# Performance work log

Hardware: AMD Instinct MI355X
Metric: run time of the kernel (lower is better)

The kernel has to match this reference:

```python
import jax, jax.numpy as jnp
import numpy as np

SEQ_LEN = 131072
NUM_NODES = 256
NUM_CAUSES = 16
NUM_FEATURES = 100
NUM_OUTPUTS = 1
NOISE_STD = 0.01


def _build_dag_mask(N, C, p, rng):
    # upper-triangular random adjacency; roots (0..C-1) have no parents;
    # every non-root gets at least one parent (mirrors _build_random_dag)
    A = (rng.random((N, N)) < p) & np.triu(np.ones((N, N), bool), k=1)
    A[:, :C] = False
    for j in range(C, N):
        if not A[:j, j].any():
            A[rng.integers(0, j), j] = True
    return A.astype(np.int32)


def setup_inputs() -> dict:
    key = jax.random.key(0)
    k1, k2, k3 = jax.random.split(key, 3)
    rng = np.random.default_rng(0)
    S, N, C = SEQ_LEN, NUM_NODES, NUM_CAUSES
    causes = jax.random.normal(k1, (S, C), dtype=jnp.float32)
    W = jax.random.normal(k2, (N, N), dtype=jnp.float32)  # edge weights w_ij ~ N(0,1)
    eps = jax.random.normal(k3, (S, N - C), dtype=jnp.float32)  # unit noise, scaled by NOISE_STD
    mask = jnp.asarray(_build_dag_mask(N, C, 0.3, rng))
    act_id = jnp.asarray(rng.integers(0, 4, size=(N - C,)), dtype=jnp.int32)
    # y from a sink-like last node; X from sorted sample of remaining non-root nodes
    y_idx = jnp.asarray([N - 1], dtype=jnp.int64)
    X_idx = jnp.asarray(np.sort(rng.choice(np.arange(C, N - 1), size=NUM_FEATURES, replace=False)), dtype=jnp.int64)
    return {"causes": causes, "W": W, "eps": eps, "mask": mask, "act_id": act_id, "X_idx": X_idx, "y_idx": y_idx}


def reference(causes, W, eps, mask, act_id, X_idx, y_idx):
    S, C = causes.shape
    N = W.shape[0]
    Wm = W * mask.astype(W.dtype)                      # [N,N] masked edge weights (parent i -> node j)
    vals0 = jnp.zeros((S, N), W.dtype).at[:, :C].set(causes)
    Wcols = Wm.T[C:]                                   # [N-C, N] incoming-weight rows per non-root node
    eps_t = eps.T                                      # [N-C, S]
    branches = [lambda z: z, jnp.tanh, jax.nn.relu, jax.nn.sigmoid]

    def step(carry, xs):
        vals, idx = carry
        w_col, e, a = xs
        z = vals @ w_col + jnp.float32(NOISE_STD) * e  # weighted parent sum + noise, [S]
        v = jax.lax.switch(a, branches, z)
        vals = vals.at[:, idx].set(v)
        return (vals, idx + 1), None

    (vals, _), _ = jax.lax.scan(step, (vals0, jnp.int32(C)), (Wcols, eps_t, act_id))
    X = vals[:, X_idx]                                 # [S, num_features]
    y = vals[:, y_idx]                                 # [S, 1]
    bad = jnp.isnan(X).any() | jnp.isnan(y).any()
    X = jnp.where(bad, jnp.float32(0.0), X)
    y = jnp.where(bad, jnp.float32(-100.0), y)
    return X, y[:, 0]                                  # num_outputs == 1 -> squeeze
```

## Files before the change

kernel.cpp:

```cpp
#include <hip/hip_runtime.h>
#include <hip/hip_bf16.h>
#include <hip/hip_fp16.h>


typedef _Float16 half8 __attribute__((ext_vector_type(8)));
typedef float    f32x4 __attribute__((ext_vector_type(4)));

constexpr int S_LEN    = 131072;
constexpr int N_NODES  = 256;
constexpr int N_CAUSES = 16;
constexpr int N_COMP   = 240;
constexpr int N_FEAT   = 100;
constexpr float NOISE  = 0.01f;
constexpr float VSC    = 0.0625f;
constexpr float VSCI   = 16.0f;

constexpr int KE_tab[16]  = {0,32,64,64,96,96,128,128,160,160,192,192,224,224,256,256};
constexpr int OFF_tab[16] = {0,0,1024,3072,5120,8192,11264,15360,19456,24576,29696,
                             35840,41984,49152,56320,64512};

__constant__ int c_KE[16]  = {0,32,64,64,96,96,128,128,160,160,192,192,224,224,256,256};
__constant__ int c_OFF[16] = {0,0,1024,3072,5120,8192,11264,15360,19456,24576,29696,
                              35840,41984,49152,56320,64512};

__device__ _Float16 g_WT[72704];
__device__ float    g_Wtri[15 * 256];

__device__ __forceinline__ bool sniff_binary64(const void* p) {
    const unsigned* u = (const unsigned*)p;
    bool ok = true;
    for (int i = 0; i < 64; ++i) ok = ok && (u[i] <= 1u);
    return ok;
}
__device__ __forceinline__ bool sniff_is_bf16(const void* p) {
    const unsigned* u = (const unsigned*)p;
    bool ok = true;
    for (int i = 0; i < 16; ++i) {
        unsigned e = ((u[i] << 16) >> 23) & 0xffu;
        ok = ok && (e >= 100u) && (e <= 132u);
    }
    return ok;
}
__device__ __forceinline__ float bflo(unsigned u) { return __uint_as_float(u << 16); }
__device__ __forceinline__ float bfhi(unsigned u) { return __uint_as_float(u & 0xffff0000u); }

__device__ __forceinline__ void load16(const void* base, long long off, bool isbf, float* o) {
    if (isbf) {
        const uint4* p = (const uint4*)((const unsigned short*)base + off);
        uint4 a = p[0], b = p[1];
        o[0]=bflo(a.x); o[1]=bfhi(a.x); o[2]=bflo(a.y); o[3]=bfhi(a.y);
        o[4]=bflo(a.z); o[5]=bfhi(a.z); o[6]=bflo(a.w); o[7]=bfhi(a.w);
        o[8]=bflo(b.x); o[9]=bfhi(b.x); o[10]=bflo(b.y); o[11]=bfhi(b.y);
        o[12]=bflo(b.z); o[13]=bfhi(b.z); o[14]=bflo(b.w); o[15]=bfhi(b.w);
    } else {
        const float4* p = (const float4*)((const float*)base + off);
        float4 x0=p[0], x1=p[1], x2=p[2], x3=p[3];
        o[0]=x0.x; o[1]=x0.y; o[2]=x0.z; o[3]=x0.w;
        o[4]=x1.x; o[5]=x1.y; o[6]=x1.z; o[7]=x1.w;
        o[8]=x2.x; o[9]=x2.y; o[10]=x2.z; o[11]=x2.w;
        o[12]=x3.x; o[13]=x3.y; o[14]=x3.z; o[15]=x3.w;
    }
}

__device__ __forceinline__ float hw_exp2(float x) {
    float r; asm("v_exp_f32 %0, %1" : "=v"(r) : "v"(x)); return r;
}
__device__ __forceinline__ float hw_rcp(float x) {
    float r; asm("v_rcp_f32 %0, %1" : "=v"(r) : "v"(x)); return r;
}
__device__ __forceinline__ float fast_tanh(float x) {
    float t = hw_exp2(x * 2.88539008177792681f);
    return 1.0f - 2.0f * hw_rcp(t + 1.0f);
}
__device__ __forceinline__ float fast_sigmoid(float x) {
    return hw_rcp(1.0f + hw_exp2(x * -1.44269504088896341f));
}

__global__ void prep_kernel(const void* __restrict__ A, const void* __restrict__ B) {
    __shared__ int s_mA, s_wbf;
    if (threadIdx.x == 0) {
        s_mA  = sniff_binary64(A) ? 1 : 0;
        s_wbf = sniff_is_bf16(s_mA ? B : A) ? 1 : 0;
    }
    __syncthreads();
    const int*  maskp = (const int*)(s_mA ? A : B);
    const void* Wp    = s_mA ? B : A;
    const int k = blockIdx.x + 1, j0 = 16 * k, KE = c_KE[k], OFF = c_OFF[k];
    const int tid = threadIdx.x;

    for (int n = 0; n < 16; ++n) {
        const int j = j0 + n;
        for (int kk = tid; kk < KE; kk += 256) {
            const int gi = kk * N_NODES + j;
            float w = 0.0f;
            if (maskp[gi])
                w = s_wbf ? __bfloat162float(((const __hip_bfloat16*)Wp)[gi])
                          : ((const float*)Wp)[gi];
            const _Float16 hi = (_Float16)w;
            const _Float16 lo = (_Float16)(w - (float)hi);
            g_WT[OFF + n * KE + kk]           = hi;
            g_WT[OFF + 16 * KE + n * KE + kk] = lo;
        }
    }
    {
        const int l = tid >> 4, i = tid & 15;
        const int gi = (j0 + l) * N_NODES + (j0 + i);
        float w = 0.0f;
        if (l < i && maskp[gi])
            w = s_wbf ? __bfloat162float(((const __hip_bfloat16*)Wp)[gi])
                      : ((const float*)Wp)[gi];
        g_Wtri[(k - 1) * 256 + tid] = w;
    }
}

#define MFMA16(a, b, c) __builtin_amdgcn_mfma_f32_16x16x32_f16((a), (b), (c), 0, 0, 0)

template<int K>
__device__ __forceinline__ void do_chunk(
    const int lane, const long long sg,
    const void* __restrict__ eps, const bool ebf,
    half8 (&vf)[2][8],
    float* __restrict__ Zbuf, _Float16* __restrict__ stag,
    const short* __restrict__ xpos, const int* __restrict__ act_id,
    float* __restrict__ wsX,
    float* __restrict__ outX, float* __restrict__ outY, const int yi)
{
    constexpr int j0  = 16 * K;
    constexpr int KE  = KE_tab[K];
    constexpr int NST = KE / 32;
    constexpr int OFF = OFF_tab[K];

    const int mrow = lane & 15;
    const int quad = lane >> 4;

    float ev[16];
    if (lane < 32)
        load16(eps, sg * (long long)N_COMP + (j0 - N_CAUSES), ebf, ev);

    const _Float16* __restrict__ bp = g_WT + OFF + mrow * KE + (quad << 3);

    f32x4 acc0h = {0.f,0.f,0.f,0.f}, acc0l = {0.f,0.f,0.f,0.f};
    f32x4 acc1h = {0.f,0.f,0.f,0.f}, acc1l = {0.f,0.f,0.f,0.f};

    #pragma unroll
    for (int t = 0; t < NST; ++t) {
        const half8 bh = *(const half8*)(bp + (t << 5));
        const half8 bl = *(const half8*)(bp + 16 * KE + (t << 5));
        acc0h = MFMA16(vf[0][t], bh, acc0h);
        acc1h = MFMA16(vf[1][t], bh, acc1h);
        acc0l = MFMA16(vf[0][t], bl, acc0l);
        acc1l = MFMA16(vf[1][t], bl, acc1l);
    }

    {
        const int r0 = quad << 2;
        #pragma unroll
        for (int r = 0; r < 4; ++r) {
            Zbuf[(r0 + r)      * 21 + mrow] = (acc0h[r] + acc0l[r]) * VSCI;
            Zbuf[(16 + r0 + r) * 21 + mrow] = (acc1h[r] + acc1l[r]) * VSCI;
        }
    }
    __builtin_amdgcn_wave_barrier();

    if (lane < 32) {
        float zz[16];
        #pragma unroll
        for (int i = 0; i < 16; ++i)
            zz[i] = Zbuf[lane * 21 + i] + NOISE * ev[i];

        const float* __restrict__ tri = g_Wtri + (K - 1) * 256;
        half8 h0, h1;
        #pragma unroll
        for (int i = 0; i < 16; ++i) {
            float z = zz[i];
            const int a = act_id[j0 - N_CAUSES + i];
            if (a == 1)      z = fast_tanh(z);
            else if (a == 2) z = fmaxf(z, 0.0f);
            else if (a == 3) z = fast_sigmoid(z);
            if (i < 8) h0[i] = (_Float16)(z * VSC);
            else       h1[i - 8] = (_Float16)(z * VSC);
            const int xp = xpos[j0 - N_CAUSES + i];
            if (xp >= 0) {
                if (wsX) wsX[(long long)xp * S_LEN + sg] = z;
                else     outX[xp] = z;
            }
            if (j0 + i == yi) outY[sg] = z;
            #pragma unroll
            for (int j = i + 1; j < 16; ++j)
                zz[j] += tri[(i << 4) + j] * z;
        }
        *(half8*)(stag + lane * 24)     = h0;
        *(half8*)(stag + lane * 24 + 8) = h1;
    }
    __builtin_amdgcn_wave_barrier();

    constexpr int TT = K >> 1;
    constexpr int HB = (K & 1) << 1;
    const int hq = lane >> 4;
    if (hq == HB || hq == HB + 1) {
        const int boff = (hq - HB) << 3;
        #pragma unroll
        for (int q = 0; q < 2; ++q)
            vf[q][TT] = *(const half8*)(stag + (q * 16 + (lane & 15)) * 24 + boff);
    }
    __builtin_amdgcn_wave_barrier();
}

__global__ __launch_bounds__(64, 4)
void scm_kernel(const void* __restrict__ causes,
                const void* __restrict__ eps,
                const int* __restrict__ act_id,
                const void* __restrict__ xidx_raw,
                const int* __restrict__ yidx_raw,
                float* __restrict__ out,
                float* __restrict__ wsX,
                long long ybase) {
    __shared__ __align__(16) float    Zbuf[32 * 21];
    __shared__ __align__(16) _Float16 stag[32 * 24];
    __shared__ short xpos[N_COMP];

    const int lane = threadIdx.x;
    const long long sg = (long long)blockIdx.x * 32 + lane;

    for (int t = lane; t < N_COMP; t += 64) xpos[t] = -1;
    const unsigned long long* x64 = (const unsigned long long*)xidx_raw;
    const int*                x32 = (const int*)xidx_raw;
    const bool is64 = ((x64[0] >> 32) == 0ull);
    __builtin_amdgcn_wave_barrier();
    for (int f = lane; f < N_FEAT; f += 64) {
        const int ix = is64 ? (int)x64[f] : x32[f];
        xpos[ix - N_CAUSES] = (short)f;
    }
    __builtin_amdgcn_wave_barrier();
    const int yi  = yidx_raw[0];
    const bool cbf = sniff_is_bf16(causes);
    const bool ebf = sniff_is_bf16(eps);

    half8 vz;
    #pragma unroll
    for (int e = 0; e < 8; ++e) vz[e] = (_Float16)0.0f;
    half8 vf[2][8];
    #pragma unroll
    for (int q = 0; q < 2; ++q) {
        #pragma unroll
        for (int t = 0; t < 8; ++t) vf[q][t] = vz;
    }

    if (lane < 32) {
        float cv[16];
        load16(causes, sg * (long long)N_CAUSES, cbf, cv);
        half8 c0, c1;
        #pragma unroll
        for (int i = 0; i < 8; ++i) {
            c0[i] = (_Float16)(cv[i] * VSC);
            c1[i] = (_Float16)(cv[8 + i] * VSC);
        }
        *(half8*)(stag + lane * 24)     = c0;
        *(half8*)(stag + lane * 24 + 8) = c1;
    }
    __builtin_amdgcn_wave_barrier();
    {
        const int hq = lane >> 4;
        if (hq < 2) {
            #pragma unroll
            for (int q = 0; q < 2; ++q)
                vf[q][0] = *(const half8*)(stag + (q * 16 + (lane & 15)) * 24 + (hq << 3));
        }
    }
    __builtin_amdgcn_wave_barrier();

    float* outX = out + sg * N_FEAT;
    float* outY = out + ybase;

    do_chunk< 1>(lane, sg, eps, ebf, vf, Zbuf, stag, xpos, act_id, wsX, outX, outY, yi);
    do_chunk< 2>(lane, sg, eps, ebf, vf, Zbuf, stag, xpos, act_id, wsX, outX, outY, yi);
    do_chunk< 3>(lane, sg, eps, ebf, vf, Zbuf, stag, xpos, act_id, wsX, outX, outY, yi);
    do_chunk< 4>(lane, sg, eps, ebf, vf, Zbuf, stag, xpos, act_id, wsX, outX, outY, yi);
    do_chunk< 5>(lane, sg, eps, ebf, vf, Zbuf, stag, xpos, act_id, wsX, outX, outY, yi);
    do_chunk< 6>(lane, sg, eps, ebf, vf, Zbuf, stag, xpos, act_id, wsX, outX, outY, yi);
    do_chunk< 7>(lane, sg, eps, ebf, vf, Zbuf, stag, xpos, act_id, wsX, outX, outY, yi);
    do_chunk< 8>(lane, sg, eps, ebf, vf, Zbuf, stag, xpos, act_id, wsX, outX, outY, yi);
    do_chunk< 9>(lane, sg, eps, ebf, vf, Zbuf, stag, xpos, act_id, wsX, outX, outY, yi);
    do_chunk<10>(lane, sg, eps, ebf, vf, Zbuf, stag, xpos, act_id, wsX, outX, outY, yi);
    do_chunk<11>(lane, sg, eps, ebf, vf, Zbuf, stag, xpos, act_id, wsX, outX, outY, yi);
    do_chunk<12>(lane, sg, eps, ebf, vf, Zbuf, stag, xpos, act_id, wsX, outX, outY, yi);
    do_chunk<13>(lane, sg, eps, ebf, vf, Zbuf, stag, xpos, act_id, wsX, outX, outY, yi);
    do_chunk<14>(lane, sg, eps, ebf, vf, Zbuf, stag, xpos, act_id, wsX, outX, outY, yi);
    do_chunk<15>(lane, sg, eps, ebf, vf, Zbuf, stag, xpos, act_id, wsX, outX, outY, yi);
}

__global__ __launch_bounds__(256)
void xpose_kernel(const float* __restrict__ ws, float* __restrict__ out) {
    __shared__ float tile[64 * 100];
    const int tid = threadIdx.x;
    const long long s0 = (long long)blockIdx.x * 64;
    const int f = tid >> 6;
    const int s = tid & 63;
    #pragma unroll
    for (int g = 0; g < 25; ++g) {
        const int ff = f + g * 4;
        tile[s * 100 + ff] = ws[(long long)ff * S_LEN + s0 + s];
    }
    __syncthreads();
    float4* o4 = (float4*)(out + s0 * N_FEAT);
    const float4* t4 = (const float4*)tile;
    #pragma unroll
    for (int g = 0; g < 7; ++g) {
        const int idx = g * 256 + tid;
        if (idx < 1600) o4[idx] = t4[idx];
    }
}

extern "C" void kernel_launch(void* const* d_in, const int* in_sizes, int n_in,
                              void* d_out, int out_size, void* d_ws, size_t ws_size,
                              hipStream_t stream) {
    int ic = 0, iw = 1, ie = 2, im = 3, ia = 4, ix = 5, iy = 6;
    int c = -1, e = -1, a = -1, x = -1, y = -1, m1 = -1, m2 = -1;
    for (int i = 0; i < n_in; ++i) {
        switch (in_sizes[i]) {
            case S_LEN * N_CAUSES:   c = i; break;
            case S_LEN * N_COMP:     e = i; break;
            case N_COMP:             a = i; break;
            case N_FEAT:             x = i; break;
            case 1:                  y = i; break;
            case N_NODES * N_NODES:  (m1 < 0 ? m1 : m2) = i; break;
        }
    }
    if (c >= 0 && e >= 0 && a >= 0 && x >= 0 && y >= 0 && m1 >= 0 && m2 >= 0) {
        ic = c; ie = e; ia = a; ix = x; iy = y; iw = m1; im = m2;
    }

    const void* causes = d_in[ic];
    const void* TA     = d_in[iw];
    const void* TB     = d_in[im];
    const void* eps    = d_in[ie];
    const int*  act_id = (const int*)d_in[ia];
    const void* xidx   = d_in[ix];
    const int*  yidx   = (const int*)d_in[iy];
    float*      out    = (float*)d_out;
    const long long ybase = (long long)out_size - S_LEN;

    const bool usews = ws_size >= (size_t)N_FEAT * S_LEN * sizeof(float);
    float* wsX = usews ? (float*)d_ws : nullptr;

    prep_kernel<<<15, 256, 0, stream>>>(TA, TB);
    scm_kernel<<<S_LEN / 32, 64, 0, stream>>>(causes, eps, act_id, xidx, yidx,
                                              out, wsX, ybase);
    if (usews)
        xpose_kernel<<<S_LEN / 64, 256, 0, stream>>>(wsX, out);
}
```

Baseline: 353.4 us.

## Roll chunk loop with padded full-width weights and vectorize transpose kernel

The 15 unrolled per-chunk template instantiations become a single rolled loop. Weights are stored in a uniform zero-padded 256-wide layout so each chunk always runs 8 MFMA steps instead of a variable count. This shrinks code size and instruction-cache pressure, at the price of extra MFMA work on zero-padded columns for early chunks. The transpose kernel now reads float4 vectors and pads its shared tile to cut bank conflicts.

```diff
diff --git a/kernel.cpp b/kernel.cpp
--- a/kernel.cpp
+++ b/kernel.cpp
@@ -15,15 +15,7 @@
 constexpr float VSC    = 0.0625f;
 constexpr float VSCI   = 16.0f;
 
-constexpr int KE_tab[16]  = {0,32,64,64,96,96,128,128,160,160,192,192,224,224,256,256};
-constexpr int OFF_tab[16] = {0,0,1024,3072,5120,8192,11264,15360,19456,24576,29696,
-                             35840,41984,49152,56320,64512};
-
-__constant__ int c_KE[16]  = {0,32,64,64,96,96,128,128,160,160,192,192,224,224,256,256};
-__constant__ int c_OFF[16] = {0,0,1024,3072,5120,8192,11264,15360,19456,24576,29696,
-                              35840,41984,49152,56320,64512};
-
-__device__ _Float16 g_WT[72704];
+__device__ _Float16 g_WT2[15 * 2 * 16 * 256];
 __device__ float    g_Wtri[15 * 256];
 
 __device__ __forceinline__ bool sniff_binary64(const void* p) {
@@ -85,22 +77,19 @@
     __syncthreads();
     const int*  maskp = (const int*)(s_mA ? A : B);
     const void* Wp    = s_mA ? B : A;
-    const int k = blockIdx.x + 1, j0 = 16 * k, KE = c_KE[k], OFF = c_OFF[k];
+    const int k = blockIdx.x + 1, j0 = 16 * k;
     const int tid = threadIdx.x;
 
     for (int n = 0; n < 16; ++n) {
-        const int j = j0 + n;
-        for (int kk = tid; kk < KE; kk += 256) {
-            const int gi = kk * N_NODES + j;
-            float w = 0.0f;
-            if (maskp[gi])
-                w = s_wbf ? __bfloat162float(((const __hip_bfloat16*)Wp)[gi])
-                          : ((const float*)Wp)[gi];
-            const _Float16 hi = (_Float16)w;
-            const _Float16 lo = (_Float16)(w - (float)hi);
-            g_WT[OFF + n * KE + kk]           = hi;
-            g_WT[OFF + 16 * KE + n * KE + kk] = lo;
-        }
+        const int gi = tid * N_NODES + (j0 + n);
+        float w = 0.0f;
+        if (maskp[gi])
+            w = s_wbf ? __bfloat162float(((const __hip_bfloat16*)Wp)[gi])
+                      : ((const float*)Wp)[gi];
+        const _Float16 hi = (_Float16)w;
+        const _Float16 lo = (_Float16)(w - (float)hi);
+        g_WT2[(k - 1) * 8192 + n * 256 + tid]        = hi;
+        g_WT2[(k - 1) * 8192 + 4096 + n * 256 + tid] = lo;
     }
     {
         const int l = tid >> 4, i = tid & 15;
@@ -114,97 +103,6 @@
 }
 
 #define MFMA16(a, b, c) __builtin_amdgcn_mfma_f32_16x16x32_f16((a), (b), (c), 0, 0, 0)
-
-template<int K>
-__device__ __forceinline__ void do_chunk(
-    const int lane, const long long sg,
-    const void* __restrict__ eps, const bool ebf,
-    half8 (&vf)[2][8],
-    float* __restrict__ Zbuf, _Float16* __restrict__ stag,
-    const short* __restrict__ xpos, const int* __restrict__ act_id,
-    float* __restrict__ wsX,
-    float* __restrict__ outX, float* __restrict__ outY, const int yi)
-{
-    constexpr int j0  = 16 * K;
-    constexpr int KE  = KE_tab[K];
-    constexpr int NST = KE / 32;
-    constexpr int OFF = OFF_tab[K];
-
-    const int mrow = lane & 15;
-    const int quad = lane >> 4;
-
-    float ev[16];
-    if (lane < 32)
-        load16(eps, sg * (long long)N_COMP + (j0 - N_CAUSES), ebf, ev);
-
-    const _Float16* __restrict__ bp = g_WT + OFF + mrow * KE + (quad << 3);
-
-    f32x4 acc0h = {0.f,0.f,0.f,0.f}, acc0l = {0.f,0.f,0.f,0.f};
-    f32x4 acc1h = {0.f,0.f,0.f,0.f}, acc1l = {0.f,0.f,0.f,0.f};
-
-    #pragma unroll
-    for (int t = 0; t < NST; ++t) {
-        const half8 bh = *(const half8*)(bp + (t << 5));
-        const half8 bl = *(const half8*)(bp + 16 * KE + (t << 5));
-        acc0h = MFMA16(vf[0][t], bh, acc0h);
-        acc1h = MFMA16(vf[1][t], bh, acc1h);
-        acc0l = MFMA16(vf[0][t], bl, acc0l);
-        acc1l = MFMA16(vf[1][t], bl, acc1l);
-    }
-
-    {
-        const int r0 = quad << 2;
-        #pragma unroll
-        for (int r = 0; r < 4; ++r) {
-            Zbuf[(r0 + r)      * 21 + mrow] = (acc0h[r] + acc0l[r]) * VSCI;
-            Zbuf[(16 + r0 + r) * 21 + mrow] = (acc1h[r] + acc1l[r]) * VSCI;
-        }
-    }
-    __builtin_amdgcn_wave_barrier();
-
-    if (lane < 32) {
-        float zz[16];
-        #pragma unroll
-        for (int i = 0; i < 16; ++i)
-            zz[i] = Zbuf[lane * 21 + i] + NOISE * ev[i];
-
-        const float* __restrict__ tri = g_Wtri + (K - 1) * 256;
-        half8 h0, h1;
-        #pragma unroll
-        for (int i = 0; i < 16; ++i) {
-            float z = zz[i];
-            const int a = act_id[j0 - N_CAUSES + i];
-            if (a == 1)      z = fast_tanh(z);
-            else if (a == 2) z = fmaxf(z, 0.0f);
-            else if (a == 3) z = fast_sigmoid(z);
-            if (i < 8) h0[i] = (_Float16)(z * VSC);
-            else       h1[i - 8] = (_Float16)(z * VSC);
-            const int xp = xpos[j0 - N_CAUSES + i];
-            if (xp >= 0) {
-                if (wsX) wsX[(long long)xp * S_LEN + sg] = z;
-                else     outX[xp] = z;
-            }
-            if (j0 + i == yi) outY[sg] = z;
-            #pragma unroll
-            for (int j = i + 1; j < 16; ++j)
-                zz[j] += tri[(i << 4) + j] * z;
-        }
-        *(half8*)(stag + lane * 24)     = h0;
-        *(half8*)(stag + lane * 24 + 8) = h1;
-    }
-    __builtin_amdgcn_wave_barrier();
-
-    constexpr int TT = K >> 1;
-    constexpr int HB = (K & 1) << 1;
-    const int hq = lane >> 4;
-    if (hq == HB || hq == HB + 1) {
-        const int boff = (hq - HB) << 3;
-        #pragma unroll
-        for (int q = 0; q < 2; ++q)
-            vf[q][TT] = *(const half8*)(stag + (q * 16 + (lane & 15)) * 24 + boff);
-    }
-    __builtin_amdgcn_wave_barrier();
-}
 
 __global__ __launch_bounds__(64, 4)
 void scm_kernel(const void* __restrict__ causes,
@@ -236,6 +134,9 @@
     const bool cbf = sniff_is_bf16(causes);
     const bool ebf = sniff_is_bf16(eps);
 
+    const int mrow = lane & 15;
+    const int quad = lane >> 4;
+
     half8 vz;
     #pragma unroll
     for (int e = 0; e < 8; ++e) vz[e] = (_Float16)0.0f;
@@ -259,55 +160,139 @@
         *(half8*)(stag + lane * 24 + 8) = c1;
     }
     __builtin_amdgcn_wave_barrier();
-    {
-        const int hq = lane >> 4;
-        if (hq < 2) {
-            #pragma unroll
-            for (int q = 0; q < 2; ++q)
-                vf[q][0] = *(const half8*)(stag + (q * 16 + (lane & 15)) * 24 + (hq << 3));
-        }
+    if (quad < 2) {
+        #pragma unroll
+        for (int q = 0; q < 2; ++q)
+            vf[q][0] = *(const half8*)(stag + (q * 16 + mrow) * 24 + (quad << 3));
     }
     __builtin_amdgcn_wave_barrier();
 
     float* outX = out + sg * N_FEAT;
     float* outY = out + ybase;
 
-    do_chunk< 1>(lane, sg, eps, ebf, vf, Zbuf, stag, xpos, act_id, wsX, outX, outY, yi);
-    do_chunk< 2>(lane, sg, eps, ebf, vf, Zbuf, stag, xpos, act_id, wsX, outX, outY, yi);
-    do_chunk< 3>(lane, sg, eps, ebf, vf, Zbuf, stag, xpos, act_id, wsX, outX, outY, yi);
-    do_chunk< 4>(lane, sg, eps, ebf, vf, Zbuf, stag, xpos, act_id, wsX, outX, outY, yi);
-    do_chunk< 5>(lane, sg, eps, ebf, vf, Zbuf, stag, xpos, act_id, wsX, outX, outY, yi);
-    do_chunk< 6>(lane, sg, eps, ebf, vf, Zbuf, stag, xpos, act_id, wsX, outX, outY, yi);
-    do_chunk< 7>(lane, sg, eps, ebf, vf, Zbuf, stag, xpos, act_id, wsX, outX, outY, yi);
-    do_chunk< 8>(lane, sg, eps, ebf, vf, Zbuf, stag, xpos, act_id, wsX, outX, outY, yi);
-    do_chunk< 9>(lane, sg, eps, ebf, vf, Zbuf, stag, xpos, act_id, wsX, outX, outY, yi);
-    do_chunk<10>(lane, sg, eps, ebf, vf, Zbuf, stag, xpos, act_id, wsX, outX, outY, yi);
-    do_chunk<11>(lane, sg, eps, ebf, vf, Zbuf, stag, xpos, act_id, wsX, outX, outY, yi);
-    do_chunk<12>(lane, sg, eps, ebf, vf, Zbuf, stag, xpos, act_id, wsX, outX, outY, yi);
-    do_chunk<13>(lane, sg, eps, ebf, vf, Zbuf, stag, xpos, act_id, wsX, outX, outY, yi);
-    do_chunk<14>(lane, sg, eps, ebf, vf, Zbuf, stag, xpos, act_id, wsX, outX, outY, yi);
-    do_chunk<15>(lane, sg, eps, ebf, vf, Zbuf, stag, xpos, act_id, wsX, outX, outY, yi);
+    #define UPD(TT, HB)                                                        \
+        if (quad == (HB) || quad == (HB) + 1) {                                \
+            const int boff = (quad - (HB)) << 3;                               \
+            vf[0][TT] = *(const half8*)(stag + mrow * 24 + boff);              \
+            vf[1][TT] = *(const half8*)(stag + (16 + mrow) * 24 + boff);       \
+        }
+
+    #pragma unroll 1
+    for (int k = 1; k <= 15; ++k) {
+        const int j0 = k << 4;
+
+        float ev[16];
+        if (lane < 32)
+            load16(eps, sg * (long long)N_COMP + (j0 - N_CAUSES), ebf, ev);
+
+        const _Float16* __restrict__ bp =
+            g_WT2 + (k - 1) * 8192 + mrow * 256 + (quad << 3);
+
+        f32x4 acc0h = {0.f,0.f,0.f,0.f}, acc0l = {0.f,0.f,0.f,0.f};
+        f32x4 acc1h = {0.f,0.f,0.f,0.f}, acc1l = {0.f,0.f,0.f,0.f};
+
+        #pragma unroll
+        for (int t = 0; t < 8; ++t) {
+            const half8 bh = *(const half8*)(bp + (t << 5));
+            const half8 bl = *(const half8*)(bp + 4096 + (t << 5));
+            acc0h = MFMA16(vf[0][t], bh, acc0h);
+            acc1h = MFMA16(vf[1][t], bh, acc1h);
+            acc0l = MFMA16(vf[0][t], bl, acc0l);
+            acc1l = MFMA16(vf[1][t], bl, acc1l);
+        }
+
+        {
+            const int r0 = quad << 2;
+            #pragma unroll
+            for (int r = 0; r < 4; ++r) {
+                Zbuf[(r0 + r)      * 21 + mrow] = (acc0h[r] + acc0l[r]) * VSCI;
+                Zbuf[(16 + r0 + r) * 21 + mrow] = (acc1h[r] + acc1l[r]) * VSCI;
+            }
+        }
+        __builtin_amdgcn_wave_barrier();
+
+        if (lane < 32) {
+            float zz[16];
+            #pragma unroll
+            for (int i = 0; i < 16; ++i)
+                zz[i] = Zbuf[lane * 21 + i] + NOISE * ev[i];
+
+            const float* __restrict__ tri = g_Wtri + (k - 1) * 256;
+            half8 h0, h1;
+            #pragma unroll
+            for (int i = 0; i < 16; ++i) {
+                float z = zz[i];
+                const int a = act_id[j0 - N_CAUSES + i];
+                if (a == 1)      z = fast_tanh(z);
+                else if (a == 2) z = fmaxf(z, 0.0f);
+                else if (a == 3) z = fast_sigmoid(z);
+                if (i < 8) h0[i] = (_Float16)(z * VSC);
+                else       h1[i - 8] = (_Float16)(z * VSC);
+                const int xp = xpos[j0 - N_CAUSES + i];
+                if (xp >= 0) {
+                    if (wsX) wsX[(long long)xp * S_LEN + sg] = z;
+                    else     outX[xp] = z;
+                }
+                if (j0 + i == yi) outY[sg] = z;
+                #pragma unroll
+                for (int j = i + 1; j < 16; ++j)
+                    zz[j] += tri[(i << 4) + j] * z;
+            }
+            *(half8*)(stag + lane * 24)     = h0;
+            *(half8*)(stag + lane * 24 + 8) = h1;
+        }
+        __builtin_amdgcn_wave_barrier();
+
+        switch (k) {
+            case  1: UPD(0, 2); break;
+            case  2: UPD(1, 0); break;
+            case  3: UPD(1, 2); break;
+            case  4: UPD(2, 0); break;
+            case  5: UPD(2, 2); break;
+            case  6: UPD(3, 0); break;
+            case  7: UPD(3, 2); break;
+            case  8: UPD(4, 0); break;
+            case  9: UPD(4, 2); break;
+            case 10: UPD(5, 0); break;
+            case 11: UPD(5, 2); break;
+            case 12: UPD(6, 0); break;
+            case 13: UPD(6, 2); break;
+            case 14: UPD(7, 0); break;
+            case 15: UPD(7, 2); break;
+        }
+        __builtin_amdgcn_wave_barrier();
+    }
+    #undef UPD
 }
 
 __global__ __launch_bounds__(256)
 void xpose_kernel(const float* __restrict__ ws, float* __restrict__ out) {
-    __shared__ float tile[64 * 100];
+    __shared__ float tile[64 * 108];
     const int tid = threadIdx.x;
     const long long s0 = (long long)blockIdx.x * 64;
-    const int f = tid >> 6;
-    const int s = tid & 63;
-    #pragma unroll
-    for (int g = 0; g < 25; ++g) {
-        const int ff = f + g * 4;
-        tile[s * 100 + ff] = ws[(long long)ff * S_LEN + s0 + s];
-    }
-    __syncthreads();
-    float4* o4 = (float4*)(out + s0 * N_FEAT);
-    const float4* t4 = (const float4*)tile;
     #pragma unroll
     for (int g = 0; g < 7; ++g) {
         const int idx = g * 256 + tid;
-        if (idx < 1600) o4[idx] = t4[idx];
+        if (idx < 1600) {
+            const int ff = idx >> 4;
+            const int sl = idx & 15;
+            const float4 v = *(const float4*)(ws + (long long)ff * S_LEN + s0 + sl * 4);
+            tile[(sl * 4 + 0) * 108 + ff] = v.x;
+            tile[(sl * 4 + 1) * 108 + ff] = v.y;
+            tile[(sl * 4 + 2) * 108 + ff] = v.z;
+            tile[(sl * 4 + 3) * 108 + ff] = v.w;
+        }
+    }
+    __syncthreads();
+    #pragma unroll
+    for (int g = 0; g < 7; ++g) {
+        const int idx = g * 256 + tid;
+        if (idx < 1600) {
+            const int s = idx / 25;
+            const int j = idx % 25;
+            const float4 v = *(const float4*)(tile + s * 108 + j * 4);
+            *(float4*)(out + (s0 + s) * N_FEAT + j * 4) = v;
+        }
     }
 }
 
```

Result: slower. 403.7 us (+14.2%).

## Pack activation/destination metadata, branchless activations, unconditional workspace stores, vectorized transpose

Applied to the files above, without the earlier changes.

Packs each node's activation id and output destination into one shared short. The workspace path now stores every node unconditionally: feature rows, the y row, or a trash row. This removes per-node branches and the y-index compare. Activations are computed branchlessly via selects, the explicit wave barriers are dropped, and the transpose kernel now uses float4 loads, a padded tile, and also copies y. The trade-off is extra work per node, since all three activations are evaluated and stores go to the trash row. It also needs a slightly larger workspace and relies on implicit ordering within a single wave.

```diff
diff --git a/kernel.cpp b/kernel.cpp
--- a/kernel.cpp
+++ b/kernel.cpp
@@ -14,6 +14,10 @@
 constexpr float NOISE  = 0.01f;
 constexpr float VSC    = 0.0625f;
 constexpr float VSCI   = 16.0f;
+
+constexpr int ROW_Y  = 100;
+constexpr int ROW_TR = 101;
+constexpr int WS_ROWS = 102;
 
 constexpr int KE_tab[16]  = {0,32,64,64,96,96,128,128,160,160,192,192,224,224,256,256};
 constexpr int OFF_tab[16] = {0,0,1024,3072,5120,8192,11264,15360,19456,24576,29696,
@@ -121,9 +125,9 @@
     const void* __restrict__ eps, const bool ebf,
     half8 (&vf)[2][8],
     float* __restrict__ Zbuf, _Float16* __restrict__ stag,
-    const short* __restrict__ xpos, const int* __restrict__ act_id,
+    const short* __restrict__ meta,
     float* __restrict__ wsX,
-    float* __restrict__ outX, float* __restrict__ outY, const int yi)
+    float* __restrict__ outX, float* __restrict__ outY)
 {
     constexpr int j0  = 16 * K;
     constexpr int KE  = KE_tab[K];
@@ -160,7 +164,6 @@
             Zbuf[(16 + r0 + r) * 21 + mrow] = (acc1h[r] + acc1l[r]) * VSCI;
         }
     }
-    __builtin_amdgcn_wave_barrier();
 
     if (lane < 32) {
         float zz[16];
@@ -170,40 +173,54 @@
 
         const float* __restrict__ tri = g_Wtri + (K - 1) * 256;
         half8 h0, h1;
-        #pragma unroll
-        for (int i = 0; i < 16; ++i) {
-            float z = zz[i];
-            const int a = act_id[j0 - N_CAUSES + i];
-            if (a == 1)      z = fast_tanh(z);
-            else if (a == 2) z = fmaxf(z, 0.0f);
-            else if (a == 3) z = fast_sigmoid(z);
-            if (i < 8) h0[i] = (_Float16)(z * VSC);
-            else       h1[i - 8] = (_Float16)(z * VSC);
-            const int xp = xpos[j0 - N_CAUSES + i];
-            if (xp >= 0) {
-                if (wsX) wsX[(long long)xp * S_LEN + sg] = z;
-                else     outX[xp] = z;
+        if (wsX) {
+            #pragma unroll
+            for (int i = 0; i < 16; ++i) {
+                float z = zz[i];
+                const int m = meta[j0 - N_CAUSES + i];
+                const int a = m & 3;
+                const float th = fast_tanh(z);
+                const float re = fmaxf(z, 0.0f);
+                const float sgm = fast_sigmoid(z);
+                z = (a == 1) ? th : (a == 2) ? re : (a == 3) ? sgm : z;
+                if (i < 8) h0[i] = (_Float16)(z * VSC);
+                else       h1[i - 8] = (_Float16)(z * VSC);
+                wsX[((long long)(m >> 2)) * S_LEN + sg] = z;
+                #pragma unroll
+                for (int j = i + 1; j < 16; ++j)
+                    zz[j] += tri[(i << 4) + j] * z;
             }
-            if (j0 + i == yi) outY[sg] = z;
+        } else {
             #pragma unroll
-            for (int j = i + 1; j < 16; ++j)
-                zz[j] += tri[(i << 4) + j] * z;
+            for (int i = 0; i < 16; ++i) {
+                float z = zz[i];
+                const int m = meta[j0 - N_CAUSES + i];
+                const int a = m & 3;
+                if (a == 1)      z = fast_tanh(z);
+                else if (a == 2) z = fmaxf(z, 0.0f);
+                else if (a == 3) z = fast_sigmoid(z);
+                if (i < 8) h0[i] = (_Float16)(z * VSC);
+                else       h1[i - 8] = (_Float16)(z * VSC);
+                const int dr = m >> 2;
+                if (dr < ROW_Y)       outX[dr] = z;
+                else if (dr == ROW_Y) outY[sg] = z;
+                #pragma unroll
+                for (int j = i + 1; j < 16; ++j)
+                    zz[j] += tri[(i << 4) + j] * z;
+            }
         }
         *(half8*)(stag + lane * 24)     = h0;
         *(half8*)(stag + lane * 24 + 8) = h1;
     }
-    __builtin_amdgcn_wave_barrier();
 
     constexpr int TT = K >> 1;
     constexpr int HB = (K & 1) << 1;
-    const int hq = lane >> 4;
-    if (hq == HB || hq == HB + 1) {
-        const int boff = (hq - HB) << 3;
+    if (quad == HB || quad == HB + 1) {
+        const int boff = (quad - HB) << 3;
         #pragma unroll
         for (int q = 0; q < 2; ++q)
-            vf[q][TT] = *(const half8*)(stag + (q * 16 + (lane & 15)) * 24 + boff);
-    }
-    __builtin_amdgcn_wave_barrier();
+            vf[q][TT] = *(const half8*)(stag + (q * 16 + mrow) * 24 + boff);
+    }
 }
 
 __global__ __launch_bounds__(64, 4)
@@ -217,24 +234,30 @@
                 long long ybase) {
     __shared__ __align__(16) float    Zbuf[32 * 21];
     __shared__ __align__(16) _Float16 stag[32 * 24];
-    __shared__ short xpos[N_COMP];
+    __shared__ short meta[N_COMP];
 
     const int lane = threadIdx.x;
     const long long sg = (long long)blockIdx.x * 32 + lane;
 
-    for (int t = lane; t < N_COMP; t += 64) xpos[t] = -1;
+    for (int t = lane; t < N_COMP; t += 64) meta[t] = -1;
     const unsigned long long* x64 = (const unsigned long long*)xidx_raw;
     const int*                x32 = (const int*)xidx_raw;
     const bool is64 = ((x64[0] >> 32) == 0ull);
-    __builtin_amdgcn_wave_barrier();
     for (int f = lane; f < N_FEAT; f += 64) {
         const int ix = is64 ? (int)x64[f] : x32[f];
-        xpos[ix - N_CAUSES] = (short)f;
-    }
-    __builtin_amdgcn_wave_barrier();
-    const int yi  = yidx_raw[0];
+        meta[ix - N_CAUSES] = (short)f;
+    }
+    const int yi = yidx_raw[0];
+    for (int n = lane; n < N_COMP; n += 64) {
+        const int xp = meta[n];
+        const int dst = (n + N_CAUSES == yi) ? ROW_Y : (xp >= 0 ? xp : ROW_TR);
+        meta[n] = (short)((act_id[n] & 3) | (dst << 2));
+    }
     const bool cbf = sniff_is_bf16(causes);
     const bool ebf = sniff_is_bf16(eps);
+
+    const int mrow = lane & 15;
+    const int quad = lane >> 4;
 
     half8 vz;
     #pragma unroll
@@ -258,56 +281,65 @@
         *(half8*)(stag + lane * 24)     = c0;
         *(half8*)(stag + lane * 24 + 8) = c1;
     }
-    __builtin_amdgcn_wave_barrier();
-    {
-        const int hq = lane >> 4;
-        if (hq < 2) {
-            #pragma unroll
-            for (int q = 0; q < 2; ++q)
-                vf[q][0] = *(const half8*)(stag + (q * 16 + (lane & 15)) * 24 + (hq << 3));
-        }
-    }
-    __builtin_amdgcn_wave_barrier();
+    if (quad < 2) {
+        #pragma unroll
+        for (int q = 0; q < 2; ++q)
+            vf[q][0] = *(const half8*)(stag + (q * 16 + mrow) * 24 + (quad << 3));
+    }
 
     float* outX = out + sg * N_FEAT;
     float* outY = out + ybase;
 
-    do_chunk< 1>(lane, sg, eps, ebf, vf, Zbuf, stag, xpos, act_id, wsX, outX, outY, yi);
-    do_chunk< 2>(lane, sg, eps, ebf, vf, Zbuf, stag, xpos, act_id, wsX, outX, outY, yi);
-    do_chunk< 3>(lane, sg, eps, ebf, vf, Zbuf, stag, xpos, act_id, wsX, outX, outY, yi);
-    do_chunk< 4>(lane, sg, eps, ebf, vf, Zbuf, stag, xpos, act_id, wsX, outX, outY, yi);
-    do_chunk< 5>(lane, sg, eps, ebf, vf, Zbuf, stag, xpos, act_id, wsX, outX, outY, yi);
-    do_chunk< 6>(lane, sg, eps, ebf, vf, Zbuf, stag, xpos, act_id, wsX, outX, outY, yi);
-    do_chunk< 7>(lane, sg, eps, ebf, vf, Zbuf, stag, xpos, act_id, wsX, outX, outY, yi);
-    do_chunk< 8>(lane, sg, eps, ebf, vf, Zbuf, stag, xpos, act_id, wsX, outX, outY, yi);
-    do_chunk< 9>(lane, sg, eps, ebf, vf, Zbuf, stag, xpos, act_id, wsX, outX, outY, yi);
-    do_chunk<10>(lane, sg, eps, ebf, vf, Zbuf, stag, xpos, act_id, wsX, outX, outY, yi);
-    do_chunk<11>(lane, sg, eps, ebf, vf, Zbuf, stag, xpos, act_id, wsX, outX, outY, yi);
-    do_chunk<12>(lane, sg, eps, ebf, vf, Zbuf, stag, xpos, act_id, wsX, outX, outY, yi);
-    do_chunk<13>(lane, sg, eps, ebf, vf, Zbuf, stag, xpos, act_id, wsX, outX, outY, yi);
-    do_chunk<14>(lane, sg, eps, ebf, vf, Zbuf, stag, xpos, act_id, wsX, outX, outY, yi);
-    do_chunk<15>(lane, sg, eps, ebf, vf, Zbuf, stag, xpos, act_id, wsX, outX, outY, yi);
+    do_chunk< 1>(lane, sg, eps, ebf, vf, Zbuf, stag, meta, wsX, outX, outY);
+    do_chunk< 2>(lane, sg, eps, ebf, vf, Zbuf, stag, meta, wsX, outX, outY);
+    do_chunk< 3>(lane, sg, eps, ebf, vf, Zbuf, stag, meta, wsX, outX, outY);
+    do_chunk< 4>(lane, sg, eps, ebf, vf, Zbuf, stag, meta, wsX, outX, outY);
+    do_chunk< 5>(lane, sg, eps, ebf, vf, Zbuf, stag, meta, wsX, outX, outY);
+    do_chunk< 6>(lane, sg, eps, ebf, vf, Zbuf, stag, meta, wsX, outX, outY);
+    do_chunk< 7>(lane, sg, eps, ebf, vf, Zbuf, stag, meta, wsX, outX, outY);
+    do_chunk< 8>(lane, sg, eps, ebf, vf, Zbuf, stag, meta, wsX, outX, outY);
+    do_chunk< 9>(lane, sg, eps, ebf, vf, Zbuf, stag, meta, wsX, outX, outY);
+    do_chunk<10>(lane, sg, eps, ebf, vf, Zbuf, stag, meta, wsX, outX, outY);
+    do_chunk<11>(lane, sg, eps, ebf, vf, Zbuf, stag, meta, wsX, outX, outY);
+    do_chunk<12>(lane, sg, eps, ebf, vf, Zbuf, stag, meta, wsX, outX, outY);
+    do_chunk<13>(lane, sg, eps, ebf, vf, Zbuf, stag, meta, wsX, outX, outY);
+    do_chunk<14>(lane, sg, eps, ebf, vf, Zbuf, stag, meta, wsX, outX, outY);
+    do_chunk<15>(lane, sg, eps, ebf, vf, Zbuf, stag, meta, wsX, outX, outY);
 }
 
 __global__ __launch_bounds__(256)
-void xpose_kernel(const float* __restrict__ ws, float* __restrict__ out) {
-    __shared__ float tile[64 * 100];
+void xpose_kernel(const float* __restrict__ ws, float* __restrict__ out,
+                  long long ybase) {
+    __shared__ float tile[64 * 108];
     const int tid = threadIdx.x;
     const long long s0 = (long long)blockIdx.x * 64;
-    const int f = tid >> 6;
-    const int s = tid & 63;
-    #pragma unroll
-    for (int g = 0; g < 25; ++g) {
-        const int ff = f + g * 4;
-        tile[s * 100 + ff] = ws[(long long)ff * S_LEN + s0 + s];
-    }
-    __syncthreads();
-    float4* o4 = (float4*)(out + s0 * N_FEAT);
-    const float4* t4 = (const float4*)tile;
     #pragma unroll
     for (int g = 0; g < 7; ++g) {
         const int idx = g * 256 + tid;
-        if (idx < 1600) o4[idx] = t4[idx];
+        if (idx < 1600) {
+            const int ff = idx >> 4;
+            const int sl = idx & 15;
+            const float4 v = *(const float4*)(ws + (long long)ff * S_LEN + s0 + sl * 4);
+            tile[(sl * 4 + 0) * 108 + ff] = v.x;
+            tile[(sl * 4 + 1) * 108 + ff] = v.y;
+            tile[(sl * 4 + 2) * 108 + ff] = v.z;
+            tile[(sl * 4 + 3) * 108 + ff] = v.w;
+        }
+    }
+    if (tid < 16) {
+        const float4 v = *(const float4*)(ws + (long long)ROW_Y * S_LEN + s0 + tid * 4);
+        *(float4*)(out + ybase + s0 + tid * 4) = v;
+    }
+    __syncthreads();
+    #pragma unroll
+    for (int g = 0; g < 7; ++g) {
+        const int idx = g * 256 + tid;
+        if (idx < 1600) {
+            const int s = idx / 25;
+            const int j = idx % 25;
+            const float4 v = *(const float4*)(tile + s * 108 + j * 4);
+            *(float4*)(out + (s0 + s) * N_FEAT + j * 4) = v;
+        }
     }
 }
 
@@ -340,12 +372,12 @@
     float*      out    = (float*)d_out;
     const long long ybase = (long long)out_size - S_LEN;
 
-    const bool usews = ws_size >= (size_t)N_FEAT * S_LEN * sizeof(float);
+    const bool usews = ws_size >= (size_t)WS_ROWS * S_LEN * sizeof(float);
     float* wsX = usews ? (float*)d_ws : nullptr;
 
     prep_kernel<<<15, 256, 0, stream>>>(TA, TB);
     scm_kernel<<<S_LEN / 32, 64, 0, stream>>>(causes, eps, act_id, xidx, yidx,
                                               out, wsX, ybase);
     if (usews)
-        xpose_kernel<<<S_LEN / 64, 256, 0, stream>>>(wsX, out);
-}
+        xpose_kernel<<<S_LEN / 64, 256, 0, stream>>>(wsX, out, ybase);
+}
```

Measured after the change: 386.2 us. 1.09x slower.

## Double-buffer next chunk's weight fragments in registers and vectorize transpose loads

Applied to the files above, without the earlier changes.

Weight fragments for the next DAG chunk are now loaded into alternating register buffers while the current chunk's MFMAs and triangular solve run, so global-load latency is hidden behind compute. Launch bounds drop from 4 to 2 waves per SIMD to leave room for the extra 32 half8 registers, which costs occupancy. The transpose kernel now reads the workspace with float4 loads and pads the shared tile to 108 columns to reduce bank conflicts.

```diff
diff --git a/kernel.cpp b/kernel.cpp
--- a/kernel.cpp
+++ b/kernel.cpp
@@ -120,6 +120,7 @@
     const int lane, const long long sg,
     const void* __restrict__ eps, const bool ebf,
     half8 (&vf)[2][8],
+    half8 (&bufA)[16], half8 (&bufB)[16],
     float* __restrict__ Zbuf, _Float16* __restrict__ stag,
     const short* __restrict__ xpos, const int* __restrict__ act_id,
     float* __restrict__ wsX,
@@ -128,28 +129,39 @@
     constexpr int j0  = 16 * K;
     constexpr int KE  = KE_tab[K];
     constexpr int NST = KE / 32;
-    constexpr int OFF = OFF_tab[K];
 
     const int mrow = lane & 15;
     const int quad = lane >> 4;
+
+    half8 (&bc)[16] = *((K & 1) ? &bufA : &bufB);
+    half8 (&bn)[16] = *((K & 1) ? &bufB : &bufA);
 
     float ev[16];
     if (lane < 32)
         load16(eps, sg * (long long)N_COMP + (j0 - N_CAUSES), ebf, ev);
 
-    const _Float16* __restrict__ bp = g_WT + OFF + mrow * KE + (quad << 3);
-
     f32x4 acc0h = {0.f,0.f,0.f,0.f}, acc0l = {0.f,0.f,0.f,0.f};
     f32x4 acc1h = {0.f,0.f,0.f,0.f}, acc1l = {0.f,0.f,0.f,0.f};
 
     #pragma unroll
     for (int t = 0; t < NST; ++t) {
-        const half8 bh = *(const half8*)(bp + (t << 5));
-        const half8 bl = *(const half8*)(bp + 16 * KE + (t << 5));
-        acc0h = MFMA16(vf[0][t], bh, acc0h);
-        acc1h = MFMA16(vf[1][t], bh, acc1h);
-        acc0l = MFMA16(vf[0][t], bl, acc0l);
-        acc1l = MFMA16(vf[1][t], bl, acc1l);
+        acc0h = MFMA16(vf[0][t], bc[t],     acc0h);
+        acc1h = MFMA16(vf[1][t], bc[t],     acc1h);
+        acc0l = MFMA16(vf[0][t], bc[8 + t], acc0l);
+        acc1l = MFMA16(vf[1][t], bc[8 + t], acc1l);
+    }
+
+    if constexpr (K < 15) {
+        constexpr int KN  = K + 1;
+        constexpr int KEn = KE_tab[KN];
+        constexpr int NSTn = KEn / 32;
+        constexpr int OFFn = OFF_tab[KN];
+        const _Float16* __restrict__ bpn = g_WT + OFFn + mrow * KEn + (quad << 3);
+        #pragma unroll
+        for (int t = 0; t < NSTn; ++t) {
+            bn[t]     = *(const half8*)(bpn + (t << 5));
+            bn[8 + t] = *(const half8*)(bpn + 16 * KEn + (t << 5));
+        }
     }
 
     {
@@ -196,17 +208,16 @@
 
     constexpr int TT = K >> 1;
     constexpr int HB = (K & 1) << 1;
-    const int hq = lane >> 4;
-    if (hq == HB || hq == HB + 1) {
-        const int boff = (hq - HB) << 3;
+    if (quad == HB || quad == HB + 1) {
+        const int boff = (quad - HB) << 3;
         #pragma unroll
         for (int q = 0; q < 2; ++q)
-            vf[q][TT] = *(const half8*)(stag + (q * 16 + (lane & 15)) * 24 + boff);
-    }
-    __builtin_amdgcn_wave_barrier();
-}
-
-__global__ __launch_bounds__(64, 4)
+            vf[q][TT] = *(const half8*)(stag + (q * 16 + mrow) * 24 + boff);
+    }
+    __builtin_amdgcn_wave_barrier();
+}
+
+__global__ __launch_bounds__(64, 2)
 void scm_kernel(const void* __restrict__ causes,
                 const void* __restrict__ eps,
                 const int* __restrict__ act_id,
@@ -236,6 +247,9 @@
     const bool cbf = sniff_is_bf16(causes);
     const bool ebf = sniff_is_bf16(eps);
 
+    const int mrow = lane & 15;
+    const int quad = lane >> 4;
+
     half8 vz;
     #pragma unroll
     for (int e = 0; e < 8; ++e) vz[e] = (_Float16)0.0f;
@@ -244,6 +258,17 @@
     for (int q = 0; q < 2; ++q) {
         #pragma unroll
         for (int t = 0; t < 8; ++t) vf[q][t] = vz;
+    }
+
+    half8 bufA[16], bufB[16];
+    #pragma unroll
+    for (int t = 0; t < 16; ++t) { bufA[t] = vz; bufB[t] = vz; }
+
+    {
+        const _Float16* __restrict__ bp1 =
+            g_WT + OFF_tab[1] + mrow * KE_tab[1] + (quad << 3);
+        bufA[0] = *(const half8*)(bp1);
+        bufA[8] = *(const half8*)(bp1 + 16 * KE_tab[1]);
     }
 
     if (lane < 32) {
@@ -259,55 +284,61 @@
         *(half8*)(stag + lane * 24 + 8) = c1;
     }
     __builtin_amdgcn_wave_barrier();
-    {
-        const int hq = lane >> 4;
-        if (hq < 2) {
-            #pragma unroll
-            for (int q = 0; q < 2; ++q)
-                vf[q][0] = *(const half8*)(stag + (q * 16 + (lane & 15)) * 24 + (hq << 3));
-        }
+    if (quad < 2) {
+        #pragma unroll
+        for (int q = 0; q < 2; ++q)
+            vf[q][0] = *(const half8*)(stag + (q * 16 + mrow) * 24 + (quad << 3));
     }
     __builtin_amdgcn_wave_barrier();
 
     float* outX = out + sg * N_FEAT;
     float* outY = out + ybase;
 
-    do_chunk< 1>(lane, sg, eps, ebf, vf, Zbuf, stag, xpos, act_id, wsX, outX, outY, yi);
-    do_chunk< 2>(lane, sg, eps, ebf, vf, Zbuf, stag, xpos, act_id, wsX, outX, outY, yi);
-    do_chunk< 3>(lane, sg, eps, ebf, vf, Zbuf, stag, xpos, act_id, wsX, outX, outY, yi);
-    do_chunk< 4>(lane, sg, eps, ebf, vf, Zbuf, stag, xpos, act_id, wsX, outX, outY, yi);
-    do_chunk< 5>(lane, sg, eps, ebf, vf, Zbuf, stag, xpos, act_id, wsX, outX, outY, yi);
-    do_chunk< 6>(lane, sg, eps, ebf, vf, Zbuf, stag, xpos, act_id, wsX, outX, outY, yi);
-    do_chunk< 7>(lane, sg, eps, ebf, vf, Zbuf, stag, xpos, act_id, wsX, outX, outY, yi);
-    do_chunk< 8>(lane, sg, eps, ebf, vf, Zbuf, stag, xpos, act_id, wsX, outX, outY, yi);
-    do_chunk< 9>(lane, sg, eps, ebf, vf, Zbuf, stag, xpos, act_id, wsX, outX, outY, yi);
-    do_chunk<10>(lane, sg, eps, ebf, vf, Zbuf, stag, xpos, act_id, wsX, outX, outY, yi);
-    do_chunk<11>(lane, sg, eps, ebf, vf, Zbuf, stag, xpos, act_id, wsX, outX, outY, yi);
-    do_chunk<12>(lane, sg, eps, ebf, vf, Zbuf, stag, xpos, act_id, wsX, outX, outY, yi);
-    do_chunk<13>(lane, sg, eps, ebf, vf, Zbuf, stag, xpos, act_id, wsX, outX, outY, yi);
-    do_chunk<14>(lane, sg, eps, ebf, vf, Zbuf, stag, xpos, act_id, wsX, outX, outY, yi);
-    do_chunk<15>(lane, sg, eps, ebf, vf, Zbuf, stag, xpos, act_id, wsX, outX, outY, yi);
+    do_chunk< 1>(lane, sg, eps, ebf, vf, bufA, bufB, Zbuf, stag, xpos, act_id, wsX, outX, outY, yi);
+    do_chunk< 2>(lane, sg, eps, ebf, vf, bufA, bufB, Zbuf, stag, xpos, act_id, wsX, outX, outY, yi);
+    do_chunk< 3>(lane, sg, eps, ebf, vf, bufA, bufB, Zbuf, stag, xpos, act_id, wsX, outX, outY, yi);
+    do_chunk< 4>(lane, sg, eps, ebf, vf, bufA, bufB, Zbuf, stag, xpos, act_id, wsX, outX, outY, yi);
+    do_chunk< 5>(lane, sg, eps, ebf, vf, bufA, bufB, Zbuf, stag, xpos, act_id, wsX, outX, outY, yi);
+    do_chunk< 6>(lane, sg, eps, ebf, vf, bufA, bufB, Zbuf, stag, xpos, act_id, wsX, outX, outY, yi);
+    do_chunk< 7>(lane, sg, eps, ebf, vf, bufA, bufB, Zbuf, stag, xpos, act_id, wsX, outX, outY, yi);
+    do_chunk< 8>(lane, sg, eps, ebf, vf, bufA, bufB, Zbuf, stag, xpos, act_id, wsX, outX, outY, yi);
+    do_chunk< 9>(lane, sg, eps, ebf, vf, bufA, bufB, Zbuf, stag, xpos, act_id, wsX, outX, outY, yi);
+    do_chunk<10>(lane, sg, eps, ebf, vf, bufA, bufB, Zbuf, stag, xpos, act_id, wsX, outX, outY, yi);
+    do_chunk<11>(lane, sg, eps, ebf, vf, bufA, bufB, Zbuf, stag, xpos, act_id, wsX, outX, outY, yi);
+    do_chunk<12>(lane, sg, eps, ebf, vf, bufA, bufB, Zbuf, stag, xpos, act_id, wsX, outX, outY, yi);
+    do_chunk<13>(lane, sg, eps, ebf, vf, bufA, bufB, Zbuf, stag, xpos, act_id, wsX, outX, outY, yi);
+    do_chunk<14>(lane, sg, eps, ebf, vf, bufA, bufB, Zbuf, stag, xpos, act_id, wsX, outX, outY, yi);
+    do_chunk<15>(lane, sg, eps, ebf, vf, bufA, bufB, Zbuf, stag, xpos, act_id, wsX, outX, outY, yi);
 }
 
 __global__ __launch_bounds__(256)
 void xpose_kernel(const float* __restrict__ ws, float* __restrict__ out) {
-    __shared__ float tile[64 * 100];
+    __shared__ float tile[64 * 108];
     const int tid = threadIdx.x;
     const long long s0 = (long long)blockIdx.x * 64;
-    const int f = tid >> 6;
-    const int s = tid & 63;
-    #pragma unroll
-    for (int g = 0; g < 25; ++g) {
-        const int ff = f + g * 4;
-        tile[s * 100 + ff] = ws[(long long)ff * S_LEN + s0 + s];
-    }
-    __syncthreads();
-    float4* o4 = (float4*)(out + s0 * N_FEAT);
-    const float4* t4 = (const float4*)tile;
     #pragma unroll
     for (int g = 0; g < 7; ++g) {
         const int idx = g * 256 + tid;
-        if (idx < 1600) o4[idx] = t4[idx];
+        if (idx < 1600) {
+            const int ff = idx >> 4;
+            const int sl = idx & 15;
+            const float4 v = *(const float4*)(ws + (long long)ff * S_LEN + s0 + sl * 4);
+            tile[(sl * 4 + 0) * 108 + ff] = v.x;
+            tile[(sl * 4 + 1) * 108 + ff] = v.y;
+            tile[(sl * 4 + 2) * 108 + ff] = v.z;
+            tile[(sl * 4 + 3) * 108 + ff] = v.w;
+        }
+    }
+    __syncthreads();
+    #pragma unroll
+    for (int g = 0; g < 7; ++g) {
+        const int idx = g * 256 + tid;
+        if (idx < 1600) {
+            const int s = idx / 25;
+            const int j = idx % 25;
+            const float4 v = *(const float4*)(tile + s * 108 + j * 4);
+            *(float4*)(out + (s0 + s) * N_FEAT + j * 4) = v;
+        }
     }
 }
 
```

After: 371.2 us. 5.0% more time.
